# Optimization experiments

Hardware: AMD Instinct MI355X
Metric: run time of the kernel (lower is better)

The kernel has to match this reference:

```python
import jax, jax.numpy as jnp
import numpy as np
import math

NUM_SLOTS = 512
DIM = 1024

def _l2norm(x, eps=1e-12):
    # matches F.normalize(p=2, dim=-1): x / max(||x||, eps)
    n = jnp.linalg.norm(x, axis=-1, keepdims=True)
    return x / jnp.maximum(n, eps)

def setup_inputs() -> dict:
    key = jax.random.key(0)
    ks = jax.random.split(key, 10)
    d = DIM
    s = 1.0 / math.sqrt(d)
    inp = {
        "mamba_states": jax.random.normal(ks[0], (8, 4096, d), dtype=jnp.float32),
        "memory": jax.random.normal(ks[1], (NUM_SLOTS, d), dtype=jnp.float32),  # stand-in for orthogonal init
        "Wq": jax.random.uniform(ks[2], (d, d), jnp.float32, -s, s),
        "bq": jax.random.uniform(ks[3], (d,), jnp.float32, -s, s),
        "Wk": jax.random.uniform(ks[4], (d, d), jnp.float32, -s, s),
        "bk": jax.random.uniform(ks[5], (d,), jnp.float32, -s, s),
        "Wv": jax.random.uniform(ks[6], (d, d), jnp.float32, -s, s),
        "bv": jax.random.uniform(ks[7], (d,), jnp.float32, -s, s),
        "Wg": jax.random.uniform(ks[8], (2 * d, d), jnp.float32, -1.0 / math.sqrt(2 * d), 1.0 / math.sqrt(2 * d)),
        "bg": jax.random.uniform(ks[9], (d,), jnp.float32, -1.0 / math.sqrt(2 * d), 1.0 / math.sqrt(2 * d)),
    }
    return inp

def reference(mamba_states, memory, Wq, bq, Wk, bk, Wv, bv, Wg, bg):
    d = mamba_states.shape[-1]
    Q = mamba_states @ Wq + bq                      # [b, s, d]
    K = memory @ Wk + bk                            # [n, d]
    V = memory @ Wv + bv                            # [n, d]
    Qn = _l2norm(Q)
    Kn = _l2norm(K)
    scores = jnp.einsum('bsd,nd->bsn', Qn, Kn) / jnp.sqrt(jnp.float32(d))
    w = jax.nn.softmax(scores, axis=-1)             # [b, s, n]
    R = jnp.einsum('bsn,nd->bsd', w, V)             # [b, s, d]
    gate_in = jnp.concatenate([mamba_states, R], axis=-1)  # [b, s, 2d]
    g = jax.nn.sigmoid(gate_in @ Wg + bg)           # [b, s, d]
    return g * mamba_states + (1.0 - g) * R
```

## Files before the change

kernel.cpp:

```cpp
#include <hip/hip_runtime.h>
#include <cstdint>

typedef __attribute__((ext_vector_type(8))) __bf16 bf16x8;
typedef __attribute__((ext_vector_type(4))) float f32x4;

__device__ __forceinline__ unsigned short f2bf(float f) {
  unsigned u = __float_as_uint(f);
  unsigned r = (u + 0x7FFFu + ((u >> 16) & 1u)) >> 16;
  return (unsigned short)r;
}
__device__ __forceinline__ float bf2f(unsigned short u) {
  return __uint_as_float(((unsigned)u) << 16);
}

__device__ __forceinline__ __attribute__((address_space(3))) void* to_lds(void* p) {
  return (__attribute__((address_space(3))) void*)p;
}
__device__ __forceinline__ const __attribute__((address_space(1))) void* to_glb(const void* p) {
  return (const __attribute__((address_space(1))) void*)p;
}

template <int OFS>
__device__ __forceinline__ bf16x8 lds_rd(unsigned a) {
  bf16x8 r;
  asm volatile("ds_read_b128 %0, %1 offset:%2" : "=v"(r) : "v"(a), "i"(OFS));
  return r;
}

__global__ void k_transpose_bf16(const float* __restrict__ in, unsigned short* __restrict__ out,
                                 int R, int C) {
  __shared__ float tile[32][33];
  int c0 = blockIdx.x * 32, r0 = blockIdx.y * 32;
  int tx = threadIdx.x, ty = threadIdx.y;
  #pragma unroll
  for (int i = 0; i < 32; i += 8)
    tile[ty + i][tx] = in[(size_t)(r0 + ty + i) * C + c0 + tx];
  __syncthreads();
  #pragma unroll
  for (int i = 0; i < 32; i += 8)
    out[(size_t)(c0 + ty + i) * R + r0 + tx] = f2bf(tile[tx][ty + i]);
}

__global__ void k_convert_bf16(const float4* __restrict__ in, ushort4* __restrict__ out, int n4) {
  int i = blockIdx.x * blockDim.x + threadIdx.x;
  if (i < n4) {
    float4 v = in[i];
    ushort4 o; o.x = f2bf(v.x); o.y = f2bf(v.y); o.z = f2bf(v.z); o.w = f2bf(v.w);
    out[i] = o;
  }
}

__global__ void k_stage_x(const float4* __restrict__ X, unsigned short* __restrict__ gate_in, int n4) {
  int i = blockIdx.x * blockDim.x + threadIdx.x;
  if (i < n4) {
    int flat = i << 2;
    int row = flat >> 10, col = flat & 1023;
    float4 v = X[i];
    ushort4 o; o.x = f2bf(v.x); o.y = f2bf(v.y); o.z = f2bf(v.z); o.w = f2bf(v.w);
    *(ushort4*)(gate_in + (size_t)row * 2048 + col) = o;
  }
}

__global__ void k_concat_bias(const float* __restrict__ bk, const float* __restrict__ bv,
                              float* __restrict__ bkv) {
  int i = blockIdx.x * blockDim.x + threadIdx.x;
  if (i < 2048) bkv[i] = (i < 1024) ? bk[i] : bv[i - 1024];
}

__global__ void k_post_kv(const float4* __restrict__ KV, unsigned short* __restrict__ Kn,
                          unsigned short* __restrict__ Vt) {
  int row = blockIdx.x;
  int tid = threadIdx.x;
  const float4* r = KV + (size_t)row * 512;
  float4 k4 = r[tid];
  float4 v4 = r[256 + tid];
  float s = k4.x * k4.x + k4.y * k4.y + k4.z * k4.z + k4.w * k4.w;
  #pragma unroll
  for (int m = 32; m; m >>= 1) s += __shfl_xor(s, m, 64);
  __shared__ float red[4];
  if ((tid & 63) == 0) red[tid >> 6] = s;
  __syncthreads();
  float tot = red[0] + red[1] + red[2] + red[3];
  float inv = 1.0f / fmaxf(sqrtf(tot), 1e-12f);
  ushort4 o; o.x = f2bf(k4.x * inv); o.y = f2bf(k4.y * inv);
  o.z = f2bf(k4.z * inv); o.w = f2bf(k4.w * inv);
  *(ushort4*)(Kn + (size_t)row * 1024 + tid * 4) = o;
  int vc = tid * 4;
  Vt[(size_t)(vc + 0) * 512 + row] = f2bf(v4.x);
  Vt[(size_t)(vc + 1) * 512 + row] = f2bf(v4.y);
  Vt[(size_t)(vc + 2) * 512 + row] = f2bf(v4.z);
  Vt[(size_t)(vc + 3) * 512 + row] = f2bf(v4.w);
}

__global__ void k_softmax(const float4* __restrict__ S, const float* __restrict__ norm2,
                          unsigned short* __restrict__ W) {
  int tid = threadIdx.x;
  int wv = tid >> 6, lane = tid & 63;
  int row = blockIdx.x * 4 + wv;
  float alpha = 0.03125f * rsqrtf(fmaxf(norm2[row], 1e-24f));
  const float4* sr = S + (size_t)row * 128;
  float4 a = sr[lane], b = sr[64 + lane];
  a.x *= alpha; a.y *= alpha; a.z *= alpha; a.w *= alpha;
  b.x *= alpha; b.y *= alpha; b.z *= alpha; b.w *= alpha;
  float m = fmaxf(fmaxf(fmaxf(a.x, a.y), fmaxf(a.z, a.w)),
                  fmaxf(fmaxf(b.x, b.y), fmaxf(b.z, b.w)));
  #pragma unroll
  for (int o = 32; o; o >>= 1) m = fmaxf(m, __shfl_xor(m, o, 64));
  a.x = __expf(a.x - m); a.y = __expf(a.y - m); a.z = __expf(a.z - m); a.w = __expf(a.w - m);
  b.x = __expf(b.x - m); b.y = __expf(b.y - m); b.z = __expf(b.z - m); b.w = __expf(b.w - m);
  float s = a.x + a.y + a.z + a.w + b.x + b.y + b.z + b.w;
  #pragma unroll
  for (int o = 32; o; o >>= 1) s += __shfl_xor(s, o, 64);
  float inv = 1.0f / s;
  ushort4 oa, ob;
  oa.x = f2bf(a.x * inv); oa.y = f2bf(a.y * inv); oa.z = f2bf(a.z * inv); oa.w = f2bf(a.w * inv);
  ob.x = f2bf(b.x * inv); ob.y = f2bf(b.y * inv); ob.z = f2bf(b.z * inv); ob.w = f2bf(b.w * inv);
  ushort4* wr = (ushort4*)(W + (size_t)row * 512);
  wr[lane] = oa; wr[64 + lane] = ob;
}

template <int MODE>
__global__ __launch_bounds__(256, 2) void k_gemm(
    const unsigned short* __restrict__ A, int lda,
    const unsigned short* __restrict__ B, int ldb,
    const float* __restrict__ bias, float scale,
    float* __restrict__ C, int ldc,
    unsigned short* __restrict__ Cb, int ldcb,
    float* __restrict__ Cnorm,
    int K) {
  __shared__ __align__(16) unsigned short As[128 * 64];
  __shared__ __align__(16) unsigned short Bs[128 * 64];
  const int tid = threadIdx.x;
  const int lane = tid & 63, w = tid >> 6;

  int mt = blockIdx.y, nt = blockIdx.x;
  const int m0 = mt * 128, n0 = nt * 128;

  const int srow = lane >> 3;
  const int schunk = (lane & 7) ^ srow;
  const unsigned short* gA = A + (size_t)(m0 + w * 8 + srow) * lda + schunk * 8;
  const unsigned short* gB = B + (size_t)(n0 + w * 8 + srow) * ldb + schunk * 8;
  unsigned short* lA = As + (w * 8) * 64;
  unsigned short* lB = Bs + (w * 8) * 64;

  f32x4 acc[4][4];
  f32x4 zero = {0.f, 0.f, 0.f, 0.f};
  #pragma unroll
  for (int i = 0; i < 4; ++i)
    #pragma unroll
    for (int j = 0; j < 4; ++j) acc[i][j] = zero;

  const int fr = lane & 15, q = lane >> 4;
  const int wr = (w >> 1) * 64, wc = (w & 1) * 64;

  for (int k0 = 0; k0 < K; k0 += 64) {
    #pragma unroll
    for (int i = 0; i < 4; ++i) {
      __builtin_amdgcn_global_load_lds(to_glb(gA + (size_t)i * 32 * lda + k0),
                                       to_lds(lA + i * 32 * 64), 16, 0, 0);
      __builtin_amdgcn_global_load_lds(to_glb(gB + (size_t)i * 32 * ldb + k0),
                                       to_lds(lB + i * 32 * 64), 16, 0, 0);
    }
    __syncthreads();
    #pragma unroll
    for (int ks = 0; ks < 2; ++ks) {
      bf16x8 af[4], bfr[4];
      const int p = (ks * 4 + q) ^ (lane & 7);
      #pragma unroll
      for (int mi = 0; mi < 4; ++mi) {
        af[mi] = *(const bf16x8*)(As + (wr + mi * 16 + fr) * 64 + p * 8);
        bfr[mi] = *(const bf16x8*)(Bs + (wc + mi * 16 + fr) * 64 + p * 8);
      }
      #pragma unroll
      for (int mi = 0; mi < 4; ++mi)
        #pragma unroll
        for (int ni = 0; ni < 4; ++ni)
          acc[mi][ni] = __builtin_amdgcn_mfma_f32_16x16x32_bf16(af[mi], bfr[ni], acc[mi][ni], 0, 0, 0);
    }
    __syncthreads();
  }

  #pragma unroll
  for (int ni = 0; ni < 4; ++ni) {
    const int gc = n0 + wc + ni * 16 + fr;
    const float bv = bias ? bias[gc] : 0.0f;
    #pragma unroll
    for (int mi = 0; mi < 4; ++mi) {
      #pragma unroll
      for (int r = 0; r < 4; ++r) {
        const int gr = m0 + wr + mi * 16 + q * 4 + r;
        float c = acc[mi][ni][r] * scale + bv;
        C[(size_t)gr * ldc + gc] = c;
      }
    }
  }
  (void)Cb; (void)ldcb; (void)Cnorm;
}

template <int MODE>
__global__ __launch_bounds__(512, 2) void k_gemm256(
    const unsigned short* __restrict__ A, int lda,
    const unsigned short* __restrict__ B, int ldb,
    const float* __restrict__ bias, float scale,
    float* __restrict__ C, int ldc,
    unsigned short* __restrict__ Cb, int ldcb,
    float* __restrict__ Cnorm,
    int K) {
  __shared__ __align__(16) unsigned short As[2 * 256 * 64];
  __shared__ __align__(16) unsigned short Bs[2 * 256 * 64];
  const int tid = threadIdx.x;
  const int lane = tid & 63, w = tid >> 6;
  const int wm = w >> 2, wn = w & 3;
  const int fr = lane & 15, q = lane >> 4;

  int mt, nt;
  {
    int f = blockIdx.y * gridDim.x + blockIdx.x;
    int NTg = gridDim.x, MTg = gridDim.y;
    if ((MTg & 7) == 0) {
      int xcd = f & 7;
      int j = f >> 3;
      nt = j % NTg;
      mt = (j / NTg) * 8 + xcd;
    } else {
      mt = blockIdx.y; nt = blockIdx.x;
    }
  }
  const int m0 = mt * 256, n0 = nt * 256;

  const int lr = lane >> 3;
  const int lc = ((lane & 7) ^ lr) * 8;
  const int NT_ = K >> 6;
  const int NITER = NT_ >> 1;

  unsigned short* As0 = As;
  unsigned short* As1 = As + 256 * 64;
  unsigned short* Bs0 = Bs;
  unsigned short* Bs1 = Bs + 256 * 64;

  const unsigned AsB = (unsigned)(size_t)to_lds(As);
  const unsigned BsB = (unsigned)(size_t)to_lds(Bs);
  const unsigned ch0 = (unsigned)((q ^ (fr & 7)) * 16);
  const unsigned vA0 = AsB + (unsigned)((wm * 64 + fr) * 128) + ch0;
  const unsigned vA1 = AsB + (unsigned)((wm * 64 + fr) * 128) + (ch0 ^ 64u);
  const unsigned vB0 = BsB + (unsigned)((wn * 32 + fr) * 128) + ch0;
  const unsigned vB1 = BsB + (unsigned)((wn * 32 + fr) * 128) + (ch0 ^ 64u);

  f32x4 acc[2][2][4][2];
  {
    f32x4 zero = {0.f, 0.f, 0.f, 0.f};
    #pragma unroll
    for (int a = 0; a < 2; ++a)
      #pragma unroll
      for (int b = 0; b < 2; ++b)
        #pragma unroll
        for (int c = 0; c < 4; ++c)
          #pragma unroll
          for (int d = 0; d < 2; ++d) acc[a][b][c][d] = zero;
  }

#define STG(g, ld, rbase, h, kt, L) do {                                        \
    int k0s = ((kt) < NT_ ? (kt) : (NT_ - 1)) * 64;                             \
    _Pragma("unroll")                                                           \
    for (int j = 0; j < 2; ++j) {                                               \
      __builtin_amdgcn_global_load_lds(                                         \
          to_glb((g) + (size_t)((rbase) + (h) * 128 + j * 64 + w * 8 + lr) *    \
                           (size_t)(ld) + k0s + lc),                            \
          to_lds((L) + ((h) * 128 + j * 64 + w * 8) * 64), 16, 0, 0);           \
    } } while (0)

#define RD_A(BUF, QM) do {                                                      \
    a_f[0][0] = lds_rd<(BUF) * 32768 + (QM) * 16384 + 0 * 2048>(vA0);           \
    a_f[0][1] = lds_rd<(BUF) * 32768 + (QM) * 16384 + 1 * 2048>(vA0);           \
    a_f[0][2] = lds_rd<(BUF) * 32768 + (QM) * 16384 + 2 * 2048>(vA0);           \
    a_f[0][3] = lds_rd<(BUF) * 32768 + (QM) * 16384 + 3 * 2048>(vA0);           \
    a_f[1][0] = lds_rd<(BUF) * 32768 + (QM) * 16384 + 0 * 2048>(vA1);           \
    a_f[1][1] = lds_rd<(BUF) * 32768 + (QM) * 16384 + 1 * 2048>(vA1);           \
    a_f[1][2] = lds_rd<(BUF) * 32768 + (QM) * 16384 + 2 * 2048>(vA1);           \
    a_f[1][3] = lds_rd<(BUF) * 32768 + (QM) * 16384 + 3 * 2048>(vA1);           \
  } while (0)

#define RD_B(BUF, QN, dst) do {                                                 \
    dst[0][0] = lds_rd<(BUF) * 32768 + (QN) * 16384 + 0 * 2048>(vB0);           \
    dst[0][1] = lds_rd<(BUF) * 32768 + (QN) * 16384 + 1 * 2048>(vB0);           \
    dst[1][0] = lds_rd<(BUF) * 32768 + (QN) * 16384 + 0 * 2048>(vB1);           \
    dst[1][1] = lds_rd<(BUF) * 32768 + (QN) * 16384 + 1 * 2048>(vB1);           \
  } while (0)

#define MQ(QM, QN, bsrc) do {                                                   \
    _Pragma("unroll")                                                           \
    for (int ks = 0; ks < 2; ++ks)                                              \
      _Pragma("unroll")                                                         \
      for (int mi = 0; mi < 4; ++mi)                                            \
        _Pragma("unroll")                                                       \
        for (int ni = 0; ni < 2; ++ni)                                          \
          acc[QM][QN][mi][ni] = __builtin_amdgcn_mfma_f32_16x16x32_bf16(        \
              a_f[ks][mi], bsrc[ks][ni], acc[QM][QN][mi][ni], 0, 0, 0);         \
  } while (0)

#define BAR_MID() do {                                                          \
    __builtin_amdgcn_s_barrier();                                               \
    asm volatile("s_waitcnt lgkmcnt(0)" ::: "memory");                          \
    __builtin_amdgcn_sched_barrier(0);                                          \
    __builtin_amdgcn_s_setprio(1);                                              \
  } while (0)

#define BAR_END() do {                                                          \
    __builtin_amdgcn_s_setprio(0);                                              \
    __builtin_amdgcn_s_barrier();                                               \
  } while (0)

#define BAR_END_VM() do {                                                       \
    __builtin_amdgcn_s_setprio(0);                                              \
    asm volatile("s_waitcnt vmcnt(6)" ::: "memory");                            \
    __builtin_amdgcn_s_barrier();                                               \
  } while (0)

  STG(A, lda, m0, 0, 0, As0);
  STG(B, ldb, n0, 0, 0, Bs0);
  STG(B, ldb, n0, 1, 0, Bs0);
  STG(A, lda, m0, 1, 0, As0);
  STG(A, lda, m0, 0, 1, As1);
  STG(B, ldb, n0, 0, 1, Bs1);
  STG(B, ldb, n0, 1, 1, Bs1);
  asm volatile("s_waitcnt vmcnt(6)" ::: "memory");
  __builtin_amdgcn_s_barrier();

  bf16x8 a_f[2][4], b0[2][2], b1[2][2];

  for (int it = 0; it < NITER; ++it) {
    const int t = it * 2;
    RD_A(0, 0); RD_B(0, 0, b0);
    STG(A, lda, m0, 1, t + 1, As1);
    BAR_MID(); MQ(0, 0, b0); BAR_END();
    RD_B(0, 1, b1);
    STG(A, lda, m0, 0, t + 2, As0);
    BAR_MID(); MQ(0, 1, b1); BAR_END();
    RD_A(0, 1);
    STG(B, ldb, n0, 0, t + 2, Bs0);
    BAR_MID(); MQ(1, 0, b0); BAR_END();
    STG(B, ldb, n0, 1, t + 2, Bs0);
    BAR_MID(); MQ(1, 1, b1); BAR_END_VM();
    RD_A(1, 0); RD_B(1, 0, b0);
    STG(A, lda, m0, 1, t + 2, As0);
    BAR_MID(); MQ(0, 0, b0); BAR_END();
    RD_B(1, 1, b1);
    STG(A, lda, m0, 0, t + 3, As1);
    BAR_MID(); MQ(0, 1, b1); BAR_END();
    RD_A(1, 1);
    STG(B, ldb, n0, 0, t + 3, Bs1);
    BAR_MID(); MQ(1, 0, b0); BAR_END();
    STG(B, ldb, n0, 1, t + 3, Bs1);
    BAR_MID(); MQ(1, 1, b1); BAR_END_VM();
  }

  asm volatile("s_waitcnt vmcnt(0)" ::: "memory");
  __builtin_amdgcn_sched_barrier(0);

#undef STG
#undef RD_A
#undef RD_B
#undef MQ
#undef BAR_MID
#undef BAR_END
#undef BAR_END_VM

  if (MODE == 1) {
    #pragma unroll
    for (int qm = 0; qm < 2; ++qm)
      #pragma unroll
      for (int mi = 0; mi < 4; ++mi) {
        float s2[4] = {0.f, 0.f, 0.f, 0.f};
        #pragma unroll
        for (int qn = 0; qn < 2; ++qn)
          #pragma unroll
          for (int ni = 0; ni < 2; ++ni) {
            const int gc = n0 + qn * 128 + wn * 32 + ni * 16 + fr;
            const float bv = bias[gc];
            #pragma unroll
            for (int r = 0; r < 4; ++r) {
              const int gr = m0 + qm * 128 + wm * 64 + mi * 16 + q * 4 + r;
              float c = acc[qm][qn][mi][ni][r] + bv;
              Cb[(size_t)gr * ldcb + gc] = f2bf(c);
              s2[r] += c * c;
            }
          }
        #pragma unroll
        for (int r = 0; r < 4; ++r) {
          float v = s2[r];
          v += __shfl_xor(v, 1, 64);
          v += __shfl_xor(v, 2, 64);
          v += __shfl_xor(v, 4, 64);
          v += __shfl_xor(v, 8, 64);
          if (fr == 0)
            atomicAdd(Cnorm + (m0 + qm * 128 + wm * 64 + mi * 16 + q * 4 + r), v);
        }
      }
  } else {
    #pragma unroll
    for (int qm = 0; qm < 2; ++qm)
      #pragma unroll
      for (int qn = 0; qn < 2; ++qn)
        #pragma unroll
        for (int ni = 0; ni < 2; ++ni) {
          const int gc = n0 + qn * 128 + wn * 32 + ni * 16 + fr;
          const float bv = bias ? bias[gc] : 0.0f;
          #pragma unroll
          for (int mi = 0; mi < 4; ++mi)
            #pragma unroll
            for (int r = 0; r < 4; ++r) {
              const int gr = m0 + qm * 128 + wm * 64 + mi * 16 + q * 4 + r;
              float c = acc[qm][qn][mi][ni][r] * scale + bv;
              if (MODE == 0) {
                C[(size_t)gr * ldc + gc] = c;
              } else if (MODE == 2) {
                Cb[(size_t)gr * ldcb + gc] = f2bf(c);
              } else {
                float g = 1.0f / (1.0f + __expf(-c));
                float x = bf2f(Cb[(size_t)gr * ldcb + gc]);
                float rr = bf2f(Cb[(size_t)gr * ldcb + 1024 + gc]);
                C[(size_t)gr * ldc + gc] = g * x + (1.0f - g) * rr;
              }
            }
        }
  }
}

extern "C" void kernel_launch(void* const* d_in, const int* in_sizes, int n_in,
                              void* d_out, int out_size, void* d_ws, size_t ws_size,
                              hipStream_t stream) {
  const float* X   = (const float*)d_in[0];
  const float* mem = (const float*)d_in[1];
  const float* Wq  = (const float*)d_in[2];
  const float* bq  = (const float*)d_in[3];
  const float* Wk  = (const float*)d_in[4];
  const float* bk  = (const float*)d_in[5];
  const float* Wv  = (const float*)d_in[6];
  const float* bv  = (const float*)d_in[7];
  const float* Wg  = (const float*)d_in[8];
  const float* bg  = (const float*)d_in[9];
  float* out = (float*)d_out;

  const int T = 32768, D = 1024, NS = 512;

  char* p = (char*)d_ws;
  auto alloc = [&](size_t b) { char* r = p; p += (b + 255) & ~(size_t)255; return r; };
  unsigned short* WqT    = (unsigned short*)alloc((size_t)D * D * 2);
  unsigned short* WkvT   = (unsigned short*)alloc((size_t)2 * D * D * 2);
  unsigned short* WgT    = (unsigned short*)alloc((size_t)D * 2 * D * 2);
  unsigned short* memb   = (unsigned short*)alloc((size_t)NS * D * 2);
  float*          bkv    = (float*)alloc((size_t)2 * D * 4);
  float*          KV     = (float*)alloc((size_t)NS * 2 * D * 4);
  unsigned short* Kn     = (unsigned short*)alloc((size_t)NS * D * 2);
  unsigned short* Vt     = (unsigned short*)alloc((size_t)D * NS * 2);
  unsigned short* gatein = (unsigned short*)alloc((size_t)T * 2 * D * 2);
  unsigned short* Qb     = (unsigned short*)alloc((size_t)T * D * 2);
  unsigned short* Wsm    = (unsigned short*)alloc((size_t)T * NS * 2);
  float*          S      = (float*)alloc((size_t)T * NS * 4);
  float*          norm2  = (float*)alloc((size_t)T * 4);

  hipMemsetAsync(norm2, 0, (size_t)T * 4, stream);

  k_transpose_bf16<<<dim3(32, 32), dim3(32, 8), 0, stream>>>(Wq, WqT, D, D);
  k_transpose_bf16<<<dim3(32, 32), dim3(32, 8), 0, stream>>>(Wk, WkvT, D, D);
  k_transpose_bf16<<<dim3(32, 32), dim3(32, 8), 0, stream>>>(Wv, WkvT + (size_t)D * D, D, D);
  k_transpose_bf16<<<dim3(32, 64), dim3(32, 8), 0, stream>>>(Wg, WgT, 2 * D, D);
  k_convert_bf16<<<512, 256, 0, stream>>>((const float4*)mem, (ushort4*)memb, NS * D / 4);
  k_concat_bias<<<8, 256, 0, stream>>>(bk, bv, bkv);
  k_stage_x<<<T * D / 4 / 256, 256, 0, stream>>>((const float4*)X, gatein, T * D / 4);

  k_gemm<0><<<dim3(2 * D / 128, NS / 128), 256, 0, stream>>>(
      memb, D, WkvT, D, bkv, 1.0f, KV, 2 * D, nullptr, 0, nullptr, D);
  k_post_kv<<<NS, 256, 0, stream>>>((const float4*)KV, Kn, Vt);

  k_gemm256<1><<<dim3(D / 256, T / 256), 512, 0, stream>>>(
      gatein, 2 * D, WqT, D, bq, 1.0f, nullptr, 0, Qb, D, norm2, D);

  k_gemm256<0><<<dim3(NS / 256, T / 256), 512, 0, stream>>>(
      Qb, D, Kn, D, nullptr, 1.0f, S, NS, nullptr, 0, nullptr, D);
  k_softmax<<<T / 4, 256, 0, stream>>>((const float4*)S, norm2, Wsm);

  k_gemm256<2><<<dim3(D / 256, T / 256), 512, 0, stream>>>(
      Wsm, NS, Vt, NS, nullptr, 1.0f, nullptr, 0, gatein + D, 2 * D, nullptr, NS);

  k_gemm256<3><<<dim3(D / 256, T / 256), 512, 0, stream>>>(
      gatein, 2 * D, WgT, 2 * D, bg, 1.0f, out, D, gatein, 2 * D, nullptr, 2 * D);

  (void)in_sizes; (void)n_in; (void)out_size; (void)ws_size;
}
```

Baseline: 610.8 us.

## Software-pipeline LDS fragment reads ahead of MFMA with one barrier per phase

Restructures the GEMM main loop so LDS fragment reads for the next sub-tile are issued before the end barrier of the current phase. The first fragment loads move outside the loop. Each phase now uses a single barrier plus a combined vmcnt/lgkmcnt wait, where before it used two barriers. This is meant to hide LDS read latency behind MFMA work and cut barrier overhead. The trade-off is tighter hazard reasoning about buffer reuse and wait counts (the prologue wait changes to vmcnt(8)), so an incorrect count could read stale data.

```diff
diff --git a/kernel.cpp b/kernel.cpp
--- a/kernel.cpp
+++ b/kernel.cpp
@@ -298,21 +298,15 @@
               a_f[ks][mi], bsrc[ks][ni], acc[QM][QN][mi][ni], 0, 0, 0);         \
   } while (0)
 
-#define BAR_MID() do {                                                          \
-    __builtin_amdgcn_s_barrier();                                               \
-    asm volatile("s_waitcnt lgkmcnt(0)" ::: "memory");                          \
+#define WAIT6() do {                                                            \
+    asm volatile("s_waitcnt vmcnt(6) lgkmcnt(0)" ::: "memory");                 \
     __builtin_amdgcn_sched_barrier(0);                                          \
-    __builtin_amdgcn_s_setprio(1);                                              \
   } while (0)
 
-#define BAR_END() do {                                                          \
-    __builtin_amdgcn_s_setprio(0);                                              \
-    __builtin_amdgcn_s_barrier();                                               \
-  } while (0)
-
-#define BAR_END_VM() do {                                                       \
-    __builtin_amdgcn_s_setprio(0);                                              \
-    asm volatile("s_waitcnt vmcnt(6)" ::: "memory");                            \
+#define FENCE() __builtin_amdgcn_sched_barrier(0)
+
+#define ENDBAR() do {                                                           \
+    __builtin_amdgcn_sched_barrier(0);                                          \
     __builtin_amdgcn_s_barrier();                                               \
   } while (0)
 
@@ -323,47 +317,89 @@
   STG(A, lda, m0, 0, 1, As1);
   STG(B, ldb, n0, 0, 1, Bs1);
   STG(B, ldb, n0, 1, 1, Bs1);
-  asm volatile("s_waitcnt vmcnt(6)" ::: "memory");
+  asm volatile("s_waitcnt vmcnt(8)" ::: "memory");
+  __builtin_amdgcn_sched_barrier(0);
   __builtin_amdgcn_s_barrier();
+  __builtin_amdgcn_sched_barrier(0);
 
   bf16x8 a_f[2][4], b0[2][2], b1[2][2];
+  RD_A(0, 0);
+  RD_B(0, 0, b0);
 
   for (int it = 0; it < NITER; ++it) {
     const int t = it * 2;
-    RD_A(0, 0); RD_B(0, 0, b0);
+    WAIT6();
+    __builtin_amdgcn_s_setprio(1);
+    RD_B(0, 1, b1);
     STG(A, lda, m0, 1, t + 1, As1);
-    BAR_MID(); MQ(0, 0, b0); BAR_END();
-    RD_B(0, 1, b1);
+    MQ(0, 0, b0);
+    __builtin_amdgcn_s_setprio(0);
+    ENDBAR();
+    WAIT6();
+    __builtin_amdgcn_s_setprio(1);
     STG(A, lda, m0, 0, t + 2, As0);
-    BAR_MID(); MQ(0, 1, b1); BAR_END();
+    MQ(0, 1, b1);
+    __builtin_amdgcn_s_setprio(0);
+    FENCE();
     RD_A(0, 1);
+    ENDBAR();
+    WAIT6();
+    __builtin_amdgcn_s_setprio(1);
     STG(B, ldb, n0, 0, t + 2, Bs0);
-    BAR_MID(); MQ(1, 0, b0); BAR_END();
+    MQ(1, 0, b0);
+    __builtin_amdgcn_s_setprio(0);
+    ENDBAR();
+    WAIT6();
+    __builtin_amdgcn_s_setprio(1);
     STG(B, ldb, n0, 1, t + 2, Bs0);
-    BAR_MID(); MQ(1, 1, b1); BAR_END_VM();
-    RD_A(1, 0); RD_B(1, 0, b0);
+    MQ(1, 1, b1);
+    __builtin_amdgcn_s_setprio(0);
+    FENCE();
+    RD_A(1, 0);
+    RD_B(1, 0, b0);
+    ENDBAR();
+    WAIT6();
+    __builtin_amdgcn_s_setprio(1);
+    RD_B(1, 1, b1);
     STG(A, lda, m0, 1, t + 2, As0);
-    BAR_MID(); MQ(0, 0, b0); BAR_END();
-    RD_B(1, 1, b1);
+    MQ(0, 0, b0);
+    __builtin_amdgcn_s_setprio(0);
+    ENDBAR();
+    WAIT6();
+    __builtin_amdgcn_s_setprio(1);
     STG(A, lda, m0, 0, t + 3, As1);
-    BAR_MID(); MQ(0, 1, b1); BAR_END();
+    MQ(0, 1, b1);
+    __builtin_amdgcn_s_setprio(0);
+    FENCE();
     RD_A(1, 1);
+    ENDBAR();
+    WAIT6();
+    __builtin_amdgcn_s_setprio(1);
     STG(B, ldb, n0, 0, t + 3, Bs1);
-    BAR_MID(); MQ(1, 0, b0); BAR_END();
+    MQ(1, 0, b0);
+    __builtin_amdgcn_s_setprio(0);
+    ENDBAR();
+    WAIT6();
+    __builtin_amdgcn_s_setprio(1);
     STG(B, ldb, n0, 1, t + 3, Bs1);
-    BAR_MID(); MQ(1, 1, b1); BAR_END_VM();
-  }
-
-  asm volatile("s_waitcnt vmcnt(0)" ::: "memory");
+    MQ(1, 1, b1);
+    __builtin_amdgcn_s_setprio(0);
+    FENCE();
+    RD_A(0, 0);
+    RD_B(0, 0, b0);
+    ENDBAR();
+  }
+
+  asm volatile("s_waitcnt vmcnt(0) lgkmcnt(0)" ::: "memory");
   __builtin_amdgcn_sched_barrier(0);
 
 #undef STG
 #undef RD_A
 #undef RD_B
 #undef MQ
-#undef BAR_MID
-#undef BAR_END
-#undef BAR_END_VM
+#undef WAIT6
+#undef FENCE
+#undef ENDBAR
 
   if (MODE == 1) {
     #pragma unroll
```

After: 597.6 us. 2.2% less time.
